# Kernel optimization log

Measured on AMD Instinct MI355X. Metric: run time of the kernel, lower is better.

The kernel has to match this reference:

```python
import jax, jax.numpy as jnp
import numpy as np

TEMP = 0.07
EPS = 1e-12  # matches torch F.normalize default eps


def _l2norm(x):
    n = jnp.sqrt(jnp.sum(x * x, axis=-1, keepdims=True))
    return x / jnp.maximum(n, EPS)


def setup_inputs() -> dict:
    key = jax.random.key(0)
    kq, kk = jax.random.split(key)
    N, D = 16384, 256
    q = jax.random.normal(kq, (N, D), dtype=jnp.float32)
    k = jax.random.normal(kk, (N, D), dtype=jnp.float32)
    return {"q": q, "k": k}


def reference(q, k):
    qn = _l2norm(q)
    kn = _l2norm(k)
    logits = (qn @ kn.T) / TEMP            # [N, N]
    # cross-entropy with labels = arange(N): mean over rows of (logsumexp - diag)
    lse = jax.nn.logsumexp(logits, axis=-1)  # [N]
    diag = jnp.diagonal(logits)              # [N]
    return jnp.mean(lse - diag)
```

## Files before the change

kernel.cpp:

```cpp
#include <hip/hip_runtime.h>
#include <hip/hip_bf16.h>
#include <cstdint>
#include <cstddef>

#define NROWS 16384
#define DDIM  256
#define SPLITS 16
#define NTILES 256

typedef __attribute__((ext_vector_type(4))) float f32x4;
typedef __attribute__((ext_vector_type(4))) float fl4;
typedef __attribute__((ext_vector_type(4))) int   i32x4;
typedef __attribute__((ext_vector_type(8))) int   i32x8;

constexpr float SCALE_EXP2 = 20.609929155556627f;
constexpr float LN2F       = 0.69314718055994531f;
constexpr float INV_T      = 14.285714285714286f;

__device__ inline void gload_lds16(const void* g, void* l) {
  __builtin_amdgcn_global_load_lds(
      (const __attribute__((address_space(1))) void*)g,
      (__attribute__((address_space(3))) void*)l, 16, 0, 0);
}

__global__ __launch_bounds__(256) void norm_kernel(
    const float* __restrict__ q, const float* __restrict__ k,
    unsigned char* __restrict__ qn, unsigned char* __restrict__ kn,
    float* __restrict__ diag, float* __restrict__ rowsum,
    float* __restrict__ out)
{
  const int wave = threadIdx.x >> 6, lane = threadIdx.x & 63;
  const int row = blockIdx.x * 4 + wave;
  const size_t off = (size_t)row * DDIM + lane * 4;

  fl4 vq = *(const fl4*)(q + off);
  fl4 vk = *(const fl4*)(k + off);
  float ssq = vq.x * vq.x + vq.y * vq.y + vq.z * vq.z + vq.w * vq.w;
  float ssk = vk.x * vk.x + vk.y * vk.y + vk.z * vk.z + vk.w * vk.w;
  float dot = vq.x * vk.x + vq.y * vk.y + vq.z * vk.z + vq.w * vk.w;
#pragma unroll
  for (int m = 1; m < 64; m <<= 1) {
    ssq += __shfl_xor(ssq, m, 64);
    ssk += __shfl_xor(ssk, m, 64);
    dot += __shfl_xor(dot, m, 64);
  }
  float rq = 1.0f / fmaxf(sqrtf(ssq), 1e-12f);
  float rk = 1.0f / fmaxf(sqrtf(ssk), 1e-12f);

  float sq = rq * SCALE_EXP2;
  int pq = __builtin_amdgcn_cvt_pk_fp8_f32(vq.x * sq, vq.y * sq, 0, false);
  pq     = __builtin_amdgcn_cvt_pk_fp8_f32(vq.z * sq, vq.w * sq, pq, true);
  *(int*)(qn + off) = pq;
  int pk = __builtin_amdgcn_cvt_pk_fp8_f32(vk.x * rk, vk.y * rk, 0, false);
  pk     = __builtin_amdgcn_cvt_pk_fp8_f32(vk.z * rk, vk.w * rk, pk, true);
  *(int*)(kn + off) = pk;

  if (lane == 0) {
    diag[row]   = dot * rq * rk * INV_T;
    rowsum[row] = 0.0f;
    if (row == 0) out[0] = 0.0f;
  }
}

__global__ __launch_bounds__(256) void lse_kernel(
    const unsigned char* __restrict__ qn, const unsigned char* __restrict__ kn,
    float* __restrict__ rowsum)
{
  __shared__ __attribute__((aligned(16))) unsigned char Bs[2][64 * DDIM];

  const int tid  = threadIdx.x;
  const int wave = tid >> 6, lane = tid & 63;
  const int l15  = lane & 15, quad = lane >> 4;
  const int split = blockIdx.x % SPLITS;
  const int rb    = blockIdx.x / SPLITS;
  const int wrow  = rb * 256 + wave * 64;
  const int t0 = (split * NTILES) / SPLITS;
  const int t1 = ((split + 1) * NTILES) / SPLITS;

  const int Ln = tid >> 4, Ljj = tid & 15;
  const int Lj = Ljj ^ Ln;
  const size_t src_off = (size_t)Ln * DDIM + (size_t)Lj * 16;

  i32x8 A[4][2];
#pragma unroll
  for (int s = 0; s < 4; ++s) {
    const unsigned char* ap = qn + (size_t)(wrow + s * 16 + l15) * DDIM + quad * 32;
#pragma unroll
    for (int ks = 0; ks < 2; ++ks)
      A[s][ks] = *(const i32x8*)(ap + ks * 128);
  }

  float sums[4][4];
#pragma unroll
  for (int s = 0; s < 4; ++s)
#pragma unroll
    for (int r = 0; r < 4; ++r) sums[s][r] = 0.0f;

  {
    const unsigned char* kbase = kn + (size_t)t0 * 64 * DDIM + src_off;
#pragma unroll
    for (int i = 0; i < 4; ++i)
      gload_lds16(kbase + i * 4096, (void*)(Bs[0] + tid * 16 + i * 4096));
  }

  for (int ct = t0; ct < t1; ++ct) {
    const int cur = (ct - t0) & 1;
    __builtin_amdgcn_s_waitcnt(0);
    __syncthreads();
    if (ct + 1 < t1) {
      const unsigned char* kbase = kn + (size_t)(ct + 1) * 64 * DDIM + src_off;
#pragma unroll
      for (int i = 0; i < 4; ++i)
        gload_lds16(kbase + i * 4096, (void*)(Bs[cur ^ 1] + tid * 16 + i * 4096));
    }

#pragma unroll
    for (int cs = 0; cs < 4; ++cs) {
      int n  = cs * 16 + l15;
      int nb = n & 15;
      const unsigned char* brow = Bs[cur] + n * DDIM;
      f32x4 acc0 = {0.f, 0.f, 0.f, 0.f};
      f32x4 acc1 = {0.f, 0.f, 0.f, 0.f};
      f32x4 acc2 = {0.f, 0.f, 0.f, 0.f};
      f32x4 acc3 = {0.f, 0.f, 0.f, 0.f};
#pragma unroll
      for (int ks = 0; ks < 2; ++ks) {
        int c0 = ks * 8 + quad * 2;
        i32x4 lo = *(const i32x4*)(brow + ((c0 ^ nb) * 16));
        i32x4 hi = *(const i32x4*)(brow + (((c0 + 1) ^ nb) * 16));
        i32x8 b = {lo.x, lo.y, lo.z, lo.w, hi.x, hi.y, hi.z, hi.w};
        acc0 = __builtin_amdgcn_mfma_scale_f32_16x16x128_f8f6f4(A[0][ks], b, acc0, 0, 0, 0, 127, 0, 127);
        acc1 = __builtin_amdgcn_mfma_scale_f32_16x16x128_f8f6f4(A[1][ks], b, acc1, 0, 0, 0, 127, 0, 127);
        acc2 = __builtin_amdgcn_mfma_scale_f32_16x16x128_f8f6f4(A[2][ks], b, acc2, 0, 0, 0, 127, 0, 127);
        acc3 = __builtin_amdgcn_mfma_scale_f32_16x16x128_f8f6f4(A[3][ks], b, acc3, 0, 0, 0, 127, 0, 127);
      }
#pragma unroll
      for (int r = 0; r < 4; ++r) {
        sums[0][r] += __builtin_amdgcn_exp2f(acc0[r]);
        sums[1][r] += __builtin_amdgcn_exp2f(acc1[r]);
        sums[2][r] += __builtin_amdgcn_exp2f(acc2[r]);
        sums[3][r] += __builtin_amdgcn_exp2f(acc3[r]);
      }
    }
  }

#pragma unroll
  for (int s = 0; s < 4; ++s)
#pragma unroll
    for (int r = 0; r < 4; ++r) {
      float v = sums[s][r];
      v += __shfl_xor(v, 1, 64);
      v += __shfl_xor(v, 2, 64);
      v += __shfl_xor(v, 4, 64);
      v += __shfl_xor(v, 8, 64);
      if (l15 == 0) atomicAdd(&rowsum[wrow + s * 16 + quad * 4 + r], v);
    }
}

__global__ void final_kernel(const float* __restrict__ rowsum,
                             const float* __restrict__ diag,
                             float* __restrict__ out)
{
  int row = blockIdx.x * 256 + threadIdx.x;
  float c = __builtin_amdgcn_logf(rowsum[row]) * LN2F - diag[row];
#pragma unroll
  for (int m = 1; m < 64; m <<= 1) c += __shfl_xor(c, m, 64);
  __shared__ float red[4];
  int wave = threadIdx.x >> 6, lane = threadIdx.x & 63;
  if (lane == 0) red[wave] = c;
  __syncthreads();
  if (threadIdx.x == 0) {
    float s = red[0] + red[1] + red[2] + red[3];
    atomicAdd(out, s * (1.0f / NROWS));
  }
}

extern "C" void kernel_launch(void* const* d_in, const int* in_sizes, int n_in,
                              void* d_out, int out_size, void* d_ws, size_t ws_size,
                              hipStream_t stream)
{
  const float* q = (const float*)d_in[0];
  const float* k = (const float*)d_in[1];
  float* out = (float*)d_out;

  char* ws = (char*)d_ws;
  unsigned char* qn = (unsigned char*)ws;
  unsigned char* kn = (unsigned char*)(ws + (4u << 20));
  float* diag   = (float*)(ws + (8u << 20));
  float* rowsum = (float*)(ws + (8u << 20) + (64u << 10));

  norm_kernel <<<NROWS / 4, 256, 0, stream>>>(q, k, qn, kn, diag, rowsum, out);
  lse_kernel  <<<(NROWS / 256) * SPLITS, 256, 0, stream>>>(qn, kn, rowsum);
  final_kernel<<<NROWS / 256, 256, 0, stream>>>(rowsum, diag, out);
}
```

Baseline: 141.2 us.

## Halve rows per wave and software-pipeline exp2 epilogue with MFMA

Each wave now handles 32 query rows instead of 64, which doubles the grid of the logsumexp kernel. The exp2 epilogue of the previous column step is interleaved with the LDS loads and MFMAs of the current step through ping-pong accumulators, seeded with -1e30 so the first epilogue contributes zero. MFMAs run under raised s_setprio, and the waitcnt is relaxed to a specific vmcnt encoding. This aims to overlap transcendental and MFMA work and improve occupancy, at the cost of reloading each K tile for twice as many row blocks.

```diff
diff --git a/kernel.cpp b/kernel.cpp
--- a/kernel.cpp
+++ b/kernel.cpp
@@ -7,6 +7,7 @@
 #define DDIM  256
 #define SPLITS 16
 #define NTILES 256
+#define TILES_PER (NTILES / SPLITS)
 
 typedef __attribute__((ext_vector_type(4))) float f32x4;
 typedef __attribute__((ext_vector_type(4))) float fl4;
@@ -73,88 +74,110 @@
   const int l15  = lane & 15, quad = lane >> 4;
   const int split = blockIdx.x % SPLITS;
   const int rb    = blockIdx.x / SPLITS;
-  const int wrow  = rb * 256 + wave * 64;
-  const int t0 = (split * NTILES) / SPLITS;
-  const int t1 = ((split + 1) * NTILES) / SPLITS;
+  const int wrow  = rb * 128 + wave * 32;
+  const int t0 = split * TILES_PER;
+  const int t1 = t0 + TILES_PER;
 
   const int Ln = tid >> 4, Ljj = tid & 15;
   const int Lj = Ljj ^ Ln;
   const size_t src_off = (size_t)Ln * DDIM + (size_t)Lj * 16;
 
-  i32x8 A[4][2];
-#pragma unroll
-  for (int s = 0; s < 4; ++s) {
-    const unsigned char* ap = qn + (size_t)(wrow + s * 16 + l15) * DDIM + quad * 32;
-#pragma unroll
-    for (int ks = 0; ks < 2; ++ks)
-      A[s][ks] = *(const i32x8*)(ap + ks * 128);
-  }
-
-  float sums[4][4];
-#pragma unroll
-  for (int s = 0; s < 4; ++s)
-#pragma unroll
-    for (int r = 0; r < 4; ++r) sums[s][r] = 0.0f;
-
+  i32x8 A00, A01, A10, A11;
   {
-    const unsigned char* kbase = kn + (size_t)t0 * 64 * DDIM + src_off;
+    const unsigned char* ap0 = qn + (size_t)(wrow + l15) * DDIM + quad * 32;
+    const unsigned char* ap1 = qn + (size_t)(wrow + 16 + l15) * DDIM + quad * 32;
+    A00 = *(const i32x8*)(ap0);
+    A01 = *(const i32x8*)(ap0 + 128);
+    A10 = *(const i32x8*)(ap1);
+    A11 = *(const i32x8*)(ap1 + 128);
+  }
+
+  const int rowoff = l15 * DDIM;
+  const int c0  = quad * 2;
+  const int o00 = rowoff + (((c0    ) ^ l15) * 16);
+  const int o01 = rowoff + (((c0 + 1) ^ l15) * 16);
+  const int o10 = rowoff + (((c0 + 8) ^ l15) * 16);
+  const int o11 = rowoff + (((c0 + 9) ^ l15) * 16);
+
+  f32x4 sums0 = {0.f, 0.f, 0.f, 0.f}, sums1 = {0.f, 0.f, 0.f, 0.f};
+  f32x4 accE0, accE1, accO0, accO1;
+  accO0 = (f32x4){-1e30f, -1e30f, -1e30f, -1e30f};
+  accO1 = accO0;
+
+  {
+    const unsigned char* kbase = kn + (size_t)t0 * (64 * DDIM) + src_off;
 #pragma unroll
     for (int i = 0; i < 4; ++i)
       gload_lds16(kbase + i * 4096, (void*)(Bs[0] + tid * 16 + i * 4096));
   }
 
+#define EPI(P0, P1) do {                                                      \
+    f32x4 e0_, e1_;                                                           \
+    e0_[0] = __builtin_amdgcn_exp2f(P0[0]);                                   \
+    e0_[1] = __builtin_amdgcn_exp2f(P0[1]);                                   \
+    e0_[2] = __builtin_amdgcn_exp2f(P0[2]);                                   \
+    e0_[3] = __builtin_amdgcn_exp2f(P0[3]);                                   \
+    e1_[0] = __builtin_amdgcn_exp2f(P1[0]);                                   \
+    e1_[1] = __builtin_amdgcn_exp2f(P1[1]);                                   \
+    e1_[2] = __builtin_amdgcn_exp2f(P1[2]);                                   \
+    e1_[3] = __builtin_amdgcn_exp2f(P1[3]);                                   \
+    sums0 += e0_;                                                             \
+    sums1 += e1_;                                                             \
+  } while (0)
+
+#define CS_STEP(C0, C1, P0, P1, BOFF) do {                                    \
+    i32x4 lo0_ = *(const i32x4*)(bb + (BOFF) + o00);                          \
+    i32x4 hi0_ = *(const i32x4*)(bb + (BOFF) + o01);                          \
+    i32x4 lo1_ = *(const i32x4*)(bb + (BOFF) + o10);                          \
+    i32x4 hi1_ = *(const i32x4*)(bb + (BOFF) + o11);                          \
+    EPI(P0, P1);                  \
+    i32x8 b0_ = {lo0_.x, lo0_.y, lo0_.z, lo0_.w, hi0_.x, hi0_.y, hi0_.z, hi0_.w}; \
+    i32x8 b1_ = {lo1_.x, lo1_.y, lo1_.z, lo1_.w, hi1_.x, hi1_.y, hi1_.z, hi1_.w}; \
+    __builtin_amdgcn_s_setprio(1);                                            \
+    C0 = __builtin_amdgcn_mfma_scale_f32_16x16x128_f8f6f4(                    \
+        A00, b0_, (f32x4){0.f, 0.f, 0.f, 0.f}, 0, 0, 0, 127, 0, 127);         \
+    C1 = __builtin_amdgcn_mfma_scale_f32_16x16x128_f8f6f4(                    \
+        A10, b0_, (f32x4){0.f, 0.f, 0.f, 0.f}, 0, 0, 0, 127, 0, 127);         \
+    C0 = __builtin_amdgcn_mfma_scale_f32_16x16x128_f8f6f4(                    \
+        A01, b1_, C0, 0, 0, 0, 127, 0, 127);                                  \
+    C1 = __builtin_amdgcn_mfma_scale_f32_16x16x128_f8f6f4(                    \
+        A11, b1_, C1, 0, 0, 0, 127, 0, 127);                                  \
+    __builtin_amdgcn_s_setprio(0);                                            \
+  } while (0)
+
   for (int ct = t0; ct < t1; ++ct) {
     const int cur = (ct - t0) & 1;
-    __builtin_amdgcn_s_waitcnt(0);
+    __builtin_amdgcn_s_waitcnt(0x0F70);
     __syncthreads();
     if (ct + 1 < t1) {
-      const unsigned char* kbase = kn + (size_t)(ct + 1) * 64 * DDIM + src_off;
+      const unsigned char* kbase = kn + (size_t)(ct + 1) * (64 * DDIM) + src_off;
 #pragma unroll
       for (int i = 0; i < 4; ++i)
         gload_lds16(kbase + i * 4096, (void*)(Bs[cur ^ 1] + tid * 16 + i * 4096));
     }
-
-#pragma unroll
-    for (int cs = 0; cs < 4; ++cs) {
-      int n  = cs * 16 + l15;
-      int nb = n & 15;
-      const unsigned char* brow = Bs[cur] + n * DDIM;
-      f32x4 acc0 = {0.f, 0.f, 0.f, 0.f};
-      f32x4 acc1 = {0.f, 0.f, 0.f, 0.f};
-      f32x4 acc2 = {0.f, 0.f, 0.f, 0.f};
-      f32x4 acc3 = {0.f, 0.f, 0.f, 0.f};
-#pragma unroll
-      for (int ks = 0; ks < 2; ++ks) {
-        int c0 = ks * 8 + quad * 2;
-        i32x4 lo = *(const i32x4*)(brow + ((c0 ^ nb) * 16));
-        i32x4 hi = *(const i32x4*)(brow + (((c0 + 1) ^ nb) * 16));
-        i32x8 b = {lo.x, lo.y, lo.z, lo.w, hi.x, hi.y, hi.z, hi.w};
-        acc0 = __builtin_amdgcn_mfma_scale_f32_16x16x128_f8f6f4(A[0][ks], b, acc0, 0, 0, 0, 127, 0, 127);
-        acc1 = __builtin_amdgcn_mfma_scale_f32_16x16x128_f8f6f4(A[1][ks], b, acc1, 0, 0, 0, 127, 0, 127);
-        acc2 = __builtin_amdgcn_mfma_scale_f32_16x16x128_f8f6f4(A[2][ks], b, acc2, 0, 0, 0, 127, 0, 127);
-        acc3 = __builtin_amdgcn_mfma_scale_f32_16x16x128_f8f6f4(A[3][ks], b, acc3, 0, 0, 0, 127, 0, 127);
-      }
-#pragma unroll
-      for (int r = 0; r < 4; ++r) {
-        sums[0][r] += __builtin_amdgcn_exp2f(acc0[r]);
-        sums[1][r] += __builtin_amdgcn_exp2f(acc1[r]);
-        sums[2][r] += __builtin_amdgcn_exp2f(acc2[r]);
-        sums[3][r] += __builtin_amdgcn_exp2f(acc3[r]);
-      }
+    const unsigned char* bb = Bs[cur];
+    CS_STEP(accE0, accE1, accO0, accO1, 0);
+    CS_STEP(accO0, accO1, accE0, accE1, 4096);
+    CS_STEP(accE0, accE1, accO0, accO1, 8192);
+    CS_STEP(accO0, accO1, accE0, accE1, 12288);
+  }
+  EPI(accO0, accO1);
+
+#undef CS_STEP
+#undef EPI
+
+#pragma unroll
+  for (int r = 0; r < 4; ++r) {
+    float v0 = sums0[r], v1 = sums1[r];
+    v0 += __shfl_xor(v0, 1, 64);  v1 += __shfl_xor(v1, 1, 64);
+    v0 += __shfl_xor(v0, 2, 64);  v1 += __shfl_xor(v1, 2, 64);
+    v0 += __shfl_xor(v0, 4, 64);  v1 += __shfl_xor(v1, 4, 64);
+    v0 += __shfl_xor(v0, 8, 64);  v1 += __shfl_xor(v1, 8, 64);
+    if (l15 == 0) {
+      atomicAdd(&rowsum[wrow + quad * 4 + r], v0);
+      atomicAdd(&rowsum[wrow + 16 + quad * 4 + r], v1);
     }
   }
-
-#pragma unroll
-  for (int s = 0; s < 4; ++s)
-#pragma unroll
-    for (int r = 0; r < 4; ++r) {
-      float v = sums[s][r];
-      v += __shfl_xor(v, 1, 64);
-      v += __shfl_xor(v, 2, 64);
-      v += __shfl_xor(v, 4, 64);
-      v += __shfl_xor(v, 8, 64);
-      if (l15 == 0) atomicAdd(&rowsum[wrow + s * 16 + quad * 4 + r], v);
-    }
 }
 
 __global__ void final_kernel(const float* __restrict__ rowsum,
@@ -190,6 +213,6 @@
   float* rowsum = (float*)(ws + (8u << 20) + (64u << 10));
 
   norm_kernel <<<NROWS / 4, 256, 0, stream>>>(q, k, qn, kn, diag, rowsum, out);
-  lse_kernel  <<<(NROWS / 256) * SPLITS, 256, 0, stream>>>(qn, kn, rowsum);
+  lse_kernel  <<<(NROWS / 128) * SPLITS, 256, 0, stream>>>(qn, kn, rowsum);
   final_kernel<<<NROWS / 256, 256, 0, stream>>>(rowsum, diag, out);
 }
```

Measured after the change: 142.8 us. Within noise of the previous version (+1.1%).
